# Optimization experiments

Hardware: AMD Instinct MI355X
Metric: run time of the kernel (lower is better)

## Reference

```python
import jax, jax.numpy as jnp
import numpy as np

NUM_HEADS = 8
NUM_GROUPS = 32
EPS = 1e-5


def setup_inputs() -> dict:
    key = jax.random.key(0)
    ks = jax.random.split(key, 5)
    B, C, H, W = 8, 512, 32, 32
    x = jax.random.normal(ks[0], (B, C, H, W), dtype=jnp.float32)
    norm_w = jnp.ones((C,), dtype=jnp.float32)
    norm_b = jnp.zeros((C,), dtype=jnp.float32)
    qkv_w = jax.random.normal(ks[1], (3 * C, C), dtype=jnp.float32) * (1.0 / np.sqrt(C))
    qkv_b = jax.random.normal(ks[2], (3 * C,), dtype=jnp.float32) * 0.02
    proj_w = jax.random.normal(ks[3], (C, C), dtype=jnp.float32) * (1.0 / np.sqrt(C))
    proj_b = jax.random.normal(ks[4], (C,), dtype=jnp.float32) * 0.02
    return {"x": x, "norm_w": norm_w, "norm_b": norm_b,
            "qkv_w": qkv_w, "qkv_b": qkv_b, "proj_w": proj_w, "proj_b": proj_b}


def _group_norm(x, w, b):
    # x: [B, C, T]; normalize over (C//G, T) per group
    B, C, T = x.shape
    xg = x.reshape(B, NUM_GROUPS, (C // NUM_GROUPS) * T)
    mean = xg.mean(axis=-1, keepdims=True)
    var = xg.var(axis=-1, keepdims=True)
    xn = ((xg - mean) * jax.lax.rsqrt(var + EPS)).reshape(B, C, T)
    return xn * w[None, :, None] + b[None, :, None]


def reference(x, norm_w, norm_b, qkv_w, qkv_b, proj_w, proj_b):
    B, C, H, W = x.shape
    T = H * W
    x3 = x.reshape(B, C, T)
    h = _group_norm(x3, norm_w, norm_b)
    # 1x1 conv == channel matmul: [B, 3C, T]
    qkv = jnp.einsum('oc,bct->bot', qkv_w, h) + qkv_b[None, :, None]
    nh = NUM_HEADS
    ch = C // nh
    qkv = qkv.reshape(B * nh, 3 * ch, T)
    q, k, v = jnp.split(qkv, 3, axis=1)  # each [B*nh, ch, T]
    scale = 1.0 / np.sqrt(np.sqrt(ch))
    w = jnp.einsum('bct,bcs->bts', q * scale, k * scale)  # [B*nh, T, T]
    w = jax.nn.softmax(w, axis=-1)
    a = jnp.einsum('bts,bcs->bct', w, v).reshape(B, C, T)
    out = jnp.einsum('oc,bct->bot', proj_w, a) + proj_b[None, :, None]
    return (x3 + out).reshape(B, C, H, W)
```

## Files before the change

### kernel.cpp

```cpp
#include <hip/hip_runtime.h>
#include <stdint.h>

typedef short v8s __attribute__((ext_vector_type(8)));
typedef float v4f __attribute__((ext_vector_type(4)));

#define MFMA(a, b, c) __builtin_amdgcn_mfma_f32_16x16x32_bf16((a), (b), (c), 0, 0, 0)

__device__ __forceinline__ short f2bf(float f) {
  union { float f; uint32_t u; } v; v.f = f;
  uint32_t r = v.u + 0x7fffu + ((v.u >> 16) & 1u);
  return (short)(r >> 16);
}

__device__ __forceinline__ uint32_t pack2(float a, float b) {
  union { float f; uint32_t u; } ua, ub; ua.f = a; ub.f = b;
  return __builtin_amdgcn_perm(ub.u, ua.u, 0x07060302u);
}

__device__ __forceinline__ void gload16(const void* g, void* l) {
  __builtin_amdgcn_global_load_lds((const __attribute__((address_space(1))) void*)g,
                                   (__attribute__((address_space(3))) void*)l,
                                   16, 0, 0);
}

__global__ __launch_bounds__(256) void prep_gn_kernel(
    const float* __restrict__ qkvw, const float* __restrict__ qkvb,
    const float* __restrict__ projw,
    short* __restrict__ Wq, short* __restrict__ Wp, float* __restrict__ bias2,
    const float* __restrict__ x, const float* __restrict__ gw,
    const float* __restrict__ gb, short* __restrict__ hT) {
  __shared__ float red[8];
  __shared__ short tile[16 * 1032];
  int tid = threadIdx.x;
  if (blockIdx.x >= 256) {
    int idx = (blockIdx.x - 256) * 256 + tid;
    if (idx < 1536 * 512) {
      int r = idx >> 9, c = idx & 511;
      int sec = r >> 9;
      int rr = r & 511;
      int nh = rr >> 6, cc = rr & 63;
      int o = nh * 192 + sec * 64 + cc;
      Wq[idx] = f2bf(qkvw[o * 512 + c]);
      if (c == 0) bias2[r] = qkvb[o];
    } else {
      int j = idx - 1536 * 512;
      if (j < 512 * 512) Wp[j] = f2bf(projw[j]);
    }
    return;
  }
  int b = blockIdx.x >> 5, g = blockIdx.x & 31;
  const float* xg = x + (b * 512 + g * 16) * 1024;
  float s = 0.f, ss = 0.f;
#pragma unroll
  for (int r = 0; r < 16; ++r) {
    float4 v = *(const float4*)(xg + r * 1024 + tid * 4);
    s += v.x + v.y + v.z + v.w;
    ss += v.x * v.x + v.y * v.y + v.z * v.z + v.w * v.w;
  }
#pragma unroll
  for (int off = 32; off > 0; off >>= 1) {
    s += __shfl_xor(s, off, 64);
    ss += __shfl_xor(ss, off, 64);
  }
  if ((tid & 63) == 0) { red[tid >> 6] = s; red[4 + (tid >> 6)] = ss; }
  __syncthreads();
  float S = red[0] + red[1] + red[2] + red[3];
  float SS = red[4] + red[5] + red[6] + red[7];
  float mean = S * (1.f / 16384.f);
  float var = SS * (1.f / 16384.f) - mean * mean;
  float inv = rsqrtf(var + 1e-5f);
#pragma unroll
  for (int r = 0; r < 16; ++r) {
    int c = g * 16 + r;
    float a = inv * gw[c];
    float bb = gb[c] - mean * a;
    float4 v = *(const float4*)(xg + r * 1024 + tid * 4);
    short* tr = tile + r * 1032 + tid * 4;
    tr[0] = f2bf(fmaf(v.x, a, bb));
    tr[1] = f2bf(fmaf(v.y, a, bb));
    tr[2] = f2bf(fmaf(v.z, a, bb));
    tr[3] = f2bf(fmaf(v.w, a, bb));
  }
  __syncthreads();
  int r = tid & 15, tq = tid >> 4;
  int c = g * 16 + r;
  short* dst = hT + b * 1024 * 512 + c;
  const short* src = tile + r * 1032;
#pragma unroll
  for (int i = 0; i < 64; ++i) {
    int t = i * 16 + tq;
    dst[t * 512] = src[t];
  }
}

__device__ __forceinline__ void gemm_k512(
    const short* __restrict__ Ag, const short* __restrict__ Bg,
    short* lA, short* lB, int wid, int lane, v4f acc[4][4]) {
  int r4 = lane >> 2, seg = lane & 3;
  int wr = (wid >> 1) * 64, wc = (wid & 1) * 64;
  int c16 = lane & 15, q8 = (lane >> 4) * 8;
  const short* ga = Ag + (wid * 16 + r4) * 512 + seg * 8;
  const short* gbp = Bg + (wid * 16 + r4) * 512 + seg * 8;
  for (int kt = 0; kt < 16; ++kt) {
    int k0 = kt * 32;
    gload16(ga + k0, lA + wid * 512);
    gload16(ga + 64 * 512 + k0, lA + (wid + 4) * 512);
    gload16(gbp + k0, lB + wid * 512);
    gload16(gbp + 64 * 512 + k0, lB + (wid + 4) * 512);
    __syncthreads();
    v8s af[4], bf[4];
#pragma unroll
    for (int i = 0; i < 4; ++i)
      af[i] = *(const v8s*)(lA + (wr + i * 16 + c16) * 32 + q8);
#pragma unroll
    for (int j = 0; j < 4; ++j)
      bf[j] = *(const v8s*)(lB + (wc + j * 16 + c16) * 32 + q8);
#pragma unroll
    for (int i = 0; i < 4; ++i)
#pragma unroll
      for (int j = 0; j < 4; ++j)
        acc[i][j] = MFMA(af[i], bf[j], acc[i][j]);
    __syncthreads();
  }
}

__global__ __launch_bounds__(256) void qkv_gemm_kernel(
    const short* __restrict__ hT, const short* __restrict__ Wq,
    const float* __restrict__ bias2,
    short* __restrict__ Qb, short* __restrict__ Kb, short* __restrict__ Vb) {
  __shared__ __align__(16) short smem[17408];
  short* lA = smem;
  short* lB = smem + 4096;
  short* vt = smem;
  int bm = blockIdx.x & 63, bo = blockIdx.x >> 6;
  int tid = threadIdx.x, wid = tid >> 6, lane = tid & 63;
  int wr = (wid >> 1) * 64, wc = (wid & 1) * 64;
  int q = lane >> 4, c16 = lane & 15;
  v4f acc[4][4];
#pragma unroll
  for (int i = 0; i < 4; ++i)
#pragma unroll
    for (int j = 0; j < 4; ++j) acc[i][j] = (v4f){0.f, 0.f, 0.f, 0.f};
  gemm_k512(hT + bm * 128 * 512, Wq + bo * 128 * 512, lA, lB, wid, lane, acc);
  float bv[4];
#pragma unroll
  for (int j = 0; j < 4; ++j) bv[j] = bias2[bo * 128 + wc + j * 16 + c16];
  if (bo < 8) {
    short* dst = (bo < 4) ? Qb : Kb;
    float sc = (bo < 4) ? 0.18033688f : 1.f;
    int obase = (bo & 3) * 128 + wc;
#pragma unroll
    for (int j = 0; j < 4; ++j) {
      int ocol = obase + j * 16 + c16;
      int nh = ocol >> 6, cc = ocol & 63;
#pragma unroll
      for (int i = 0; i < 4; ++i)
#pragma unroll
        for (int rr = 0; rr < 4; ++rr) {
          int n = bm * 128 + wr + i * 16 + q * 4 + rr;
          int b_ = n >> 10, t = n & 1023;
          float v = (acc[i][j][rr] + bv[j]) * sc;
          dst[b_ * 524288 + nh * 65536 + t * 64 + cc] = f2bf(v);
        }
    }
  } else {
#pragma unroll
    for (int j = 0; j < 4; ++j) {
      int ol = wc + j * 16 + c16;
#pragma unroll
      for (int i = 0; i < 4; ++i)
#pragma unroll
        for (int rr = 0; rr < 4; ++rr) {
          int nl = wr + i * 16 + q * 4 + rr;
          vt[ol * 136 + nl] = f2bf(acc[i][j][rr] + bv[j]);
        }
    }
    __syncthreads();
    int ol = tid >> 1, hf = tid & 1;
    int ovg = (bo - 8) * 128 + ol;
    const short* src = vt + ol * 136 + hf * 64;
    short* dstv = Vb + ovg * 8192 + bm * 128 + hf * 64;
#pragma unroll
    for (int m = 0; m < 8; ++m)
      *(v8s*)(dstv + m * 8) = *(const v8s*)(src + m * 8);
  }
}

__global__ __launch_bounds__(512, 4) void attn_kernel(
    const short* __restrict__ Qb, const short* __restrict__ Kb,
    const short* __restrict__ Vb, short* __restrict__ aT) {
  __shared__ __align__(16) short pb[8 * 32 * 76];
  int hb = blockIdx.x >> 3, tt = blockIdx.x & 7;
  int b = hb >> 3, nh = hb & 7;
  int tid = threadIdx.x, wid = tid >> 6, lane = tid & 63;
  int chunk = wid >> 2, w4 = wid & 3;
  int q = lane >> 4, c16 = lane & 15;
  const short* Qh = Qb + hb * 65536;
  const short* Kh = Kb + hb * 65536;
  const short* Vh = Vb + nh * 64 * 8192 + b * 1024;
  int t0 = tt * 128 + w4 * 32;
  int sbase = chunk * 512;
  v8s qf[2][2];
#pragma unroll
  for (int i = 0; i < 2; ++i)
#pragma unroll
    for (int kk = 0; kk < 2; ++kk)
      qf[i][kk] = *(const v8s*)(Qh + (t0 + i * 16 + c16) * 64 + kk * 32 + q * 8);
  v4f of[2][4];
  float lsum[2] = {0.f, 0.f};
#pragma unroll
  for (int i = 0; i < 2; ++i)
#pragma unroll
    for (int j = 0; j < 4; ++j) of[i][j] = (v4f){0.f, 0.f, 0.f, 0.f};
  short* pw = pb + wid * 2432;
#pragma unroll 1
  for (int st = 0; st < 8; ++st) {
    int s0 = sbase + st * 64;
    v8s kf[4][2];
#pragma unroll
    for (int j = 0; j < 4; ++j)
#pragma unroll
      for (int kk = 0; kk < 2; ++kk)
        kf[j][kk] = *(const v8s*)(Kh + (s0 + j * 16 + c16) * 64 + kk * 32 + q * 8);
#pragma unroll
    for (int j = 0; j < 4; ++j) {
      v4f s0v = (v4f){0.f, 0.f, 0.f, 0.f};
      s0v = MFMA(kf[j][0], qf[0][0], s0v);
      s0v = MFMA(kf[j][1], qf[0][1], s0v);
      v4f s1v = (v4f){0.f, 0.f, 0.f, 0.f};
      s1v = MFMA(kf[j][0], qf[1][0], s1v);
      s1v = MFMA(kf[j][1], qf[1][1], s1v);
      float p00 = __builtin_amdgcn_exp2f(s0v[0]);
      float p01 = __builtin_amdgcn_exp2f(s0v[1]);
      float p02 = __builtin_amdgcn_exp2f(s0v[2]);
      float p03 = __builtin_amdgcn_exp2f(s0v[3]);
      lsum[0] += (p00 + p01) + (p02 + p03);
      uint2 pk0;
      pk0.x = pack2(p00, p01);
      pk0.y = pack2(p02, p03);
      *(uint2*)(pw + c16 * 76 + j * 16 + q * 4) = pk0;
      float p10 = __builtin_amdgcn_exp2f(s1v[0]);
      float p11 = __builtin_amdgcn_exp2f(s1v[1]);
      float p12 = __builtin_amdgcn_exp2f(s1v[2]);
      float p13 = __builtin_amdgcn_exp2f(s1v[3]);
      lsum[1] += (p10 + p11) + (p12 + p13);
      uint2 pk1;
      pk1.x = pack2(p10, p11);
      pk1.y = pack2(p12, p13);
      *(uint2*)(pw + (16 + c16) * 76 + j * 16 + q * 4) = pk1;
    }
    v8s vf[4][2];
#pragma unroll
    for (int j = 0; j < 4; ++j)
#pragma unroll
      for (int kk = 0; kk < 2; ++kk)
        vf[j][kk] = *(const v8s*)(Vh + (j * 16 + c16) * 8192 + s0 + kk * 32 + q * 8);
    asm volatile("s_waitcnt lgkmcnt(0)" ::: "memory");
    v8s pa[2][2];
#pragma unroll
    for (int i = 0; i < 2; ++i)
#pragma unroll
      for (int kk = 0; kk < 2; ++kk)
        pa[i][kk] = *(const v8s*)(pw + (i * 16 + c16) * 76 + kk * 32 + q * 8);
#pragma unroll
    for (int i = 0; i < 2; ++i)
#pragma unroll
      for (int j = 0; j < 4; ++j) {
        of[i][j] = MFMA(pa[i][0], vf[j][0], of[i][j]);
        of[i][j] = MFMA(pa[i][1], vf[j][1], of[i][j]);
      }
  }
#pragma unroll
  for (int i = 0; i < 2; ++i) {
    lsum[i] += __shfl_xor(lsum[i], 16, 64);
    lsum[i] += __shfl_xor(lsum[i], 32, 64);
  }
  float* ex = (float*)pb + w4 * 2144;
  __syncthreads();
  if (chunk == 1) {
#pragma unroll
    for (int i = 0; i < 2; ++i) {
#pragma unroll
      for (int j = 0; j < 4; ++j)
#pragma unroll
        for (int rr = 0; rr < 4; ++rr)
          ex[(i * 16 + q * 4 + rr) * 66 + j * 16 + c16] = of[i][j][rr];
      if (q == 0) ex[2112 + i * 16 + c16] = lsum[i];
    }
  }
  __syncthreads();
  if (chunk == 0) {
    short* base = aT + b * 1024 * 512 + nh * 64;
#pragma unroll
    for (int i = 0; i < 2; ++i)
#pragma unroll
      for (int rr = 0; rr < 4; ++rr) {
        int row = i * 16 + q * 4 + rr;
        float inv = 1.f / (__shfl(lsum[i], q * 4 + rr, 64) + ex[2112 + row]);
        int t = t0 + row;
#pragma unroll
        for (int j = 0; j < 4; ++j) {
          float v = (of[i][j][rr] + ex[row * 66 + j * 16 + c16]) * inv;
          base[t * 512 + j * 16 + c16] = f2bf(v);
        }
      }
  }
}

__global__ __launch_bounds__(256) void proj_gemm_kernel(
    const short* __restrict__ Wp, const short* __restrict__ aT,
    const float* __restrict__ pbias, const float* __restrict__ x,
    float* __restrict__ out) {
  __shared__ __align__(16) short smem[8192];
  short* lA = smem;
  short* lB = smem + 4096;
  int bm = blockIdx.x & 3, bn = blockIdx.x >> 2;
  int tid = threadIdx.x, wid = tid >> 6, lane = tid & 63;
  int wr = (wid >> 1) * 64, wc = (wid & 1) * 64;
  int q = lane >> 4, c16 = lane & 15;
  v4f acc[4][4];
#pragma unroll
  for (int i = 0; i < 4; ++i)
#pragma unroll
    for (int j = 0; j < 4; ++j) acc[i][j] = (v4f){0.f, 0.f, 0.f, 0.f};
  gemm_k512(Wp + bm * 128 * 512, aT + bn * 128 * 512, lA, lB, wid, lane, acc);
  int colOff[4];
#pragma unroll
  for (int j = 0; j < 4; ++j) {
    int n = bn * 128 + wc + j * 16 + c16;
    colOff[j] = (n >> 10) * 524288 + (n & 1023);
  }
#pragma unroll
  for (int i = 0; i < 4; ++i)
#pragma unroll
    for (int rr = 0; rr < 4; ++rr) {
      int o = bm * 128 + wr + i * 16 + q * 4 + rr;
      float bs = pbias[o];
      int ro = o * 1024;
#pragma unroll
      for (int j = 0; j < 4; ++j) {
        int a = colOff[j] + ro;
        out[a] = acc[i][j][rr] + bs + x[a];
      }
    }
}

extern "C" void kernel_launch(void* const* d_in, const int* in_sizes, int n_in,
                              void* d_out, int out_size, void* d_ws, size_t ws_size,
                              hipStream_t stream) {
  const float* x = (const float*)d_in[0];
  const float* nw = (const float*)d_in[1];
  const float* nb = (const float*)d_in[2];
  const float* qkvw = (const float*)d_in[3];
  const float* qkvb = (const float*)d_in[4];
  const float* projw = (const float*)d_in[5];
  const float* projb = (const float*)d_in[6];
  float* out = (float*)d_out;
  char* w = (char*)d_ws;
  short* hT = (short*)(w);
  short* aT = (short*)(w + 8388608);
  short* Qb = (short*)(w + 16777216);
  short* Kb = (short*)(w + 25165824);
  short* Vb = (short*)(w + 33554432);
  short* Wq2 = (short*)(w + 41943040);
  short* Wp2 = (short*)(w + 43515904);
  float* b2 = (float*)(w + 44040192);

  hipLaunchKernelGGL(prep_gn_kernel, dim3(4352), dim3(256), 0, stream,
                     qkvw, qkvb, projw, Wq2, Wp2, b2, x, nw, nb, hT);
  hipLaunchKernelGGL(qkv_gemm_kernel, dim3(768), dim3(256), 0, stream,
                     hT, Wq2, b2, Qb, Kb, Vb);
  hipLaunchKernelGGL(attn_kernel, dim3(512), dim3(512), 0, stream, Qb, Kb, Vb, aT);
  hipLaunchKernelGGL(proj_gemm_kernel, dim3(256), dim3(256), 0, stream,
                     Wp2, aT, projb, x, out);
}
```

Baseline: 188.3 us.

## Stage K and V tiles cooperatively in swizzled LDS via global_load_lds

In the attention kernel, each wave used to read its own K and V fragments straight from global memory, so the four waves sharing a key chunk fetched the same data four times. Now the waves of each chunk load the 64-key K and V tiles once into LDS with direct global-to-LDS loads. Rows use an XOR swizzle, and waves read their MFMA fragments from LDS. This adds two block-wide barriers per iteration with no double buffering. It also roughly doubles the block's LDS footprint, which may stop the requested four blocks per CU from fitting.

```diff
diff --git a/kernel.cpp b/kernel.cpp
--- a/kernel.cpp
+++ b/kernel.cpp
@@ -189,7 +189,7 @@
 __global__ __launch_bounds__(512, 4) void attn_kernel(
     const short* __restrict__ Qb, const short* __restrict__ Kb,
     const short* __restrict__ Vb, short* __restrict__ aT) {
-  __shared__ __align__(16) short pb[8 * 32 * 76];
+  __shared__ __align__(16) short lds[35840];
   int hb = blockIdx.x >> 3, tt = blockIdx.x & 7;
   int b = hb >> 3, nh = hb & 7;
   int tid = threadIdx.x, wid = tid >> 6, lane = tid & 63;
@@ -200,6 +200,9 @@
   const short* Vh = Vb + nh * 64 * 8192 + b * 1024;
   int t0 = tt * 128 + w4 * 32;
   int sbase = chunk * 512;
+  short* Kst = lds + chunk * 4096;
+  short* Vst = lds + 8192 + chunk * 4096;
+  short* pw = lds + 16384 + wid * 2432;
   v8s qf[2][2];
 #pragma unroll
   for (int i = 0; i < 2; ++i)
@@ -212,16 +215,28 @@
   for (int i = 0; i < 2; ++i)
 #pragma unroll
     for (int j = 0; j < 4; ++j) of[i][j] = (v4f){0.f, 0.f, 0.f, 0.f};
-  short* pw = pb + wid * 2432;
+  int sidx0 = w4 * 128 + lane;
+  int sidx1 = w4 * 128 + 64 + lane;
+  int r0 = sidx0 >> 3, m0 = (sidx0 & 7) ^ (r0 & 7);
+  int r1 = sidx1 >> 3, m1 = (sidx1 & 7) ^ (r1 & 7);
 #pragma unroll 1
   for (int st = 0; st < 8; ++st) {
     int s0 = sbase + st * 64;
+    gload16(Kh + (s0 + r0) * 64 + m0 * 8, Kst + (w4 * 128) * 8);
+    gload16(Kh + (s0 + r1) * 64 + m1 * 8, Kst + (w4 * 128 + 64) * 8);
+    gload16(Vh + r0 * 8192 + s0 + m0 * 8, Vst + (w4 * 128) * 8);
+    gload16(Vh + r1 * 8192 + s0 + m1 * 8, Vst + (w4 * 128 + 64) * 8);
+    __syncthreads();
     v8s kf[4][2];
 #pragma unroll
-    for (int j = 0; j < 4; ++j)
-#pragma unroll
-      for (int kk = 0; kk < 2; ++kk)
-        kf[j][kk] = *(const v8s*)(Kh + (s0 + j * 16 + c16) * 64 + kk * 32 + q * 8);
+    for (int j = 0; j < 4; ++j) {
+      int row = j * 16 + c16;
+#pragma unroll
+      for (int kk = 0; kk < 2; ++kk) {
+        int pc = (kk * 4 + q) ^ (c16 & 7);
+        kf[j][kk] = *(const v8s*)(Kst + row * 64 + pc * 8);
+      }
+    }
 #pragma unroll
     for (int j = 0; j < 4; ++j) {
       v4f s0v = (v4f){0.f, 0.f, 0.f, 0.f};
@@ -251,10 +266,14 @@
     }
     v8s vf[4][2];
 #pragma unroll
-    for (int j = 0; j < 4; ++j)
-#pragma unroll
-      for (int kk = 0; kk < 2; ++kk)
-        vf[j][kk] = *(const v8s*)(Vh + (j * 16 + c16) * 8192 + s0 + kk * 32 + q * 8);
+    for (int j = 0; j < 4; ++j) {
+      int row = j * 16 + c16;
+#pragma unroll
+      for (int kk = 0; kk < 2; ++kk) {
+        int pc = (kk * 4 + q) ^ (c16 & 7);
+        vf[j][kk] = *(const v8s*)(Vst + row * 64 + pc * 8);
+      }
+    }
     asm volatile("s_waitcnt lgkmcnt(0)" ::: "memory");
     v8s pa[2][2];
 #pragma unroll
@@ -269,13 +288,14 @@
         of[i][j] = MFMA(pa[i][0], vf[j][0], of[i][j]);
         of[i][j] = MFMA(pa[i][1], vf[j][1], of[i][j]);
       }
+    __syncthreads();
   }
 #pragma unroll
   for (int i = 0; i < 2; ++i) {
     lsum[i] += __shfl_xor(lsum[i], 16, 64);
     lsum[i] += __shfl_xor(lsum[i], 32, 64);
   }
-  float* ex = (float*)pb + w4 * 2144;
+  float* ex = (float*)(lds + 16384) + w4 * 2144;
   __syncthreads();
   if (chunk == 1) {
 #pragma unroll
```

New measurement: 163.1 us. 13.4% less time.
